# Optimization experiments

Measured on AMD Instinct MI355X. Metric: run time of the kernel, lower is better.

Reference implementation:

```python
import jax, jax.numpy as jnp
import numpy as np

N_NODES = 50000
N_EDGES = 800000
N_GRAPHS = 50
N_OBS = 4
N_FEAT = 64
N_LAYERS = 3


def setup_inputs() -> dict:
    key = jax.random.key(0)
    ks = jax.random.split(key, 12)
    x = jax.random.normal(ks[0], (N_NODES, N_OBS), dtype=jnp.float32)
    # every node appears at least once as a target (col) so degree > 0 everywhere
    row = jax.random.randint(ks[1], (N_EDGES,), 0, N_NODES, dtype=jnp.int32)
    col = jnp.concatenate([
        jnp.arange(N_NODES, dtype=jnp.int32),
        jax.random.randint(ks[2], (N_EDGES - N_NODES,), 0, N_NODES, dtype=jnp.int32),
    ])
    edge_index = jnp.stack([row, col])  # [2, E]
    batch = jnp.repeat(jnp.arange(N_GRAPHS, dtype=jnp.int32), N_NODES // N_GRAPHS)

    def w(k, shape):
        fan_in = shape[0]
        return jax.random.normal(k, shape, dtype=jnp.float32) / jnp.sqrt(jnp.float32(fan_in))

    return {
        "x": x,
        "W_init": w(ks[3], (N_OBS, N_FEAT)),
        "W_e1": w(ks[4], (N_OBS, N_FEAT - 1)),
        "W_e2": w(ks[5], (N_FEAT, N_FEAT)),
        "W_msg": w(ks[6], (N_LAYERS, 2 * N_FEAT, N_FEAT)),
        "W_upd": w(ks[7], (N_LAYERS, 2 * N_FEAT, N_FEAT)),
        "W_pool": w(ks[8], (N_FEAT, N_FEAT)),
        "W_read": w(ks[9], (2 * N_FEAT, 1)),
        "b_read": jnp.zeros((1,), dtype=jnp.float32),
        "edge_index": edge_index,
        "batch": batch,
        "batch_size": N_GRAPHS,
    }


def reference(x, W_init, W_e1, W_e2, W_msg, W_upd, W_pool, W_read, b_read,
              edge_index, batch, batch_size):
    n = x.shape[0]
    row, col = edge_index[0], edge_index[1]
    # in-degree at target nodes (PyG degree(col, N))
    deg = jax.ops.segment_sum(jnp.ones_like(col, dtype=x.dtype), col, num_segments=n)
    deg_inv = (1.0 / deg)[:, None]  # [N,1]

    # node init embedding
    cur = jax.nn.relu(x @ W_init)  # [N,F]

    # EdgeAndNodeEmbeddingLayer
    h = jax.nn.relu(x @ W_e1)  # [N,F-1]
    agg = deg_inv * jax.ops.segment_sum(h[row], col, num_segments=n)  # [N,F-1]
    y = jnp.concatenate([agg, (deg / deg.max())[:, None]], axis=1)  # [N,F]
    edge_emb = jax.nn.relu(y @ W_e2)  # [N,F]

    # UpdateNodeEmbeddingLayer x n_layers
    for i in range(W_msg.shape[0]):
        nagg = deg_inv * jax.ops.segment_sum(cur[row], col, num_segments=n)
        msg = jax.nn.relu(jnp.concatenate([nagg, edge_emb], axis=-1) @ W_msg[i])
        cur = jax.nn.relu(jnp.concatenate([cur, msg], axis=-1) @ W_upd[i])

    # ReadoutLayer (graphs are equal-sized, batch is sorted -> means[batch])
    counts = jax.ops.segment_sum(jnp.ones((n,), dtype=x.dtype), batch, num_segments=batch_size)
    means = jax.ops.segment_sum(cur, batch, num_segments=batch_size) / counts[:, None]
    global_pool = means[batch]  # [N,F]
    f_pooled = global_pool @ W_pool
    features = jax.nn.relu(jnp.concatenate([f_pooled, cur], axis=-1))  # [N,2F]
    out = features @ W_read + b_read  # [N,1]
    return out
```

## Files before the change

### kernel.cpp

```cpp
#include <hip/hip_runtime.h>
#include <hip/hip_bf16.h>

#define N_NODES 50000
#define N_EDGES 800000
#define NF      64
#define NG      50
#define NPG     (N_NODES / NG)
#define SCAN_NBLK ((N_NODES + 255) / 256)
#define MCHUNK  20
#define MROWS   (NPG / MCHUNK)
#define NTILES  (N_NODES / 16)
#define GATHER_BLKS ((NTILES + 3) / 4)
#define INIT_BLKS ((N_NODES * 32 + 255) / 256)
#define NBKT ((N_NODES + 255) / 256)
#define BKT_CAP 6144
#define P1_EPB 4096
#define P1_BLKS ((N_EDGES + P1_EPB - 1) / P1_EPB)

typedef __attribute__((ext_vector_type(8))) short bf16x8;
typedef __attribute__((ext_vector_type(4))) float f32x4;
typedef unsigned short u16;
typedef unsigned char u8;

__device__ inline unsigned pkbf(float a, float b) {
    unsigned ua = __float_as_uint(a) + 0x8000u;
    unsigned ub = __float_as_uint(b) + 0x8000u;
    return (ua >> 16) | (ub & 0xFFFF0000u);
}
__device__ inline short bf1(float a) {
    return (short)((__float_as_uint(a) + 0x8000u) >> 16);
}
__device__ inline float lo2f(unsigned u) { return __uint_as_float(u << 16); }
__device__ inline float hi2f(unsigned u) { return __uint_as_float(u & 0xFFFF0000u); }
__device__ inline void accp(float2* a, uint4 v) {
    a[0].x += lo2f(v.x); a[0].y += hi2f(v.x);
    a[1].x += lo2f(v.y); a[1].y += hi2f(v.y);
    a[2].x += lo2f(v.z); a[2].y += hi2f(v.z);
    a[3].x += lo2f(v.w); a[3].y += hi2f(v.w);
}

__global__ void k_bucket_init(const int* __restrict__ row, const int* __restrict__ col,
                              int* __restrict__ bktCnt, unsigned* __restrict__ bktData,
                              const float* __restrict__ x, const float* __restrict__ Wi,
                              const float* __restrict__ We1,
                              u16* __restrict__ cur, u16* __restrict__ h) {
    if (blockIdx.x < P1_BLKS) {
        __shared__ int lh[256], lbase[256];
        int t = threadIdx.x;
        lh[t] = 0;
        __syncthreads();
        int e0 = blockIdx.x * P1_EPB;
        int myb[16], myr[16];
        unsigned mypk[16];
#pragma unroll
        for (int i = 0; i < 16; i++) {
            int e = e0 + i * 256 + t;
            myb[i] = -1;
            if (e < N_EDGES) {
                int c = col[e];
                mypk[i] = ((unsigned)c << 16) | (unsigned)row[e];
                int b = c >> 8;
                myb[i] = b;
                myr[i] = atomicAdd(&lh[b], 1);
            }
        }
        __syncthreads();
        if (lh[t] > 0) lbase[t] = atomicAdd(&bktCnt[t], lh[t]);
        __syncthreads();
#pragma unroll
        for (int i = 0; i < 16; i++)
            if (myb[i] >= 0)
                bktData[(size_t)myb[i] * BKT_CAP + lbase[myb[i]] + myr[i]] = mypk[i];
        return;
    }
    int idx = (blockIdx.x - P1_BLKS) * 256 + threadIdx.x;
    int node = idx >> 5, q = idx & 31;
    if (node >= N_NODES) return;
    int f0 = 2 * q, f1 = 2 * q + 1;
    float4 xv = ((const float4*)x)[node];
    float c0 = xv.x * Wi[f0] + xv.y * Wi[64 + f0] + xv.z * Wi[128 + f0] + xv.w * Wi[192 + f0];
    float c1 = xv.x * Wi[f1] + xv.y * Wi[64 + f1] + xv.z * Wi[128 + f1] + xv.w * Wi[192 + f1];
    ((unsigned*)cur)[node * 32 + q] = pkbf(fmaxf(c0, 0.f), fmaxf(c1, 0.f));
    float h0 = xv.x * We1[f0] + xv.y * We1[63 + f0] + xv.z * We1[126 + f0] + xv.w * We1[189 + f0];
    h0 = fmaxf(h0, 0.f);
    float h1 = 0.f;
    if (f1 < 63) {
        h1 = xv.x * We1[f1] + xv.y * We1[63 + f1] + xv.z * We1[126 + f1] + xv.w * We1[189 + f1];
        h1 = fmaxf(h1, 0.f);
    }
    ((unsigned*)h)[node * 32 + q] = pkbf(h0, h1);
}

__global__ __launch_bounds__(256) void k_bsort(
        const unsigned* __restrict__ bktData, const int* __restrict__ bktCnt,
        int* __restrict__ deg, int* __restrict__ rowptr, u16* __restrict__ csr) {
    int b = blockIdx.x, t = threadIdx.x;
    int cnt = bktCnt[b];
    int p = (t < b) ? bktCnt[t] : 0;
    for (int off = 32; off; off >>= 1) p += __shfl_xor(p, off, 64);
    __shared__ int sr[4];
    if ((t & 63) == 0) sr[t >> 6] = p;
    __shared__ int lh[256];
    lh[t] = 0;
    __syncthreads();
    int prev = sr[0] + sr[1] + sr[2] + sr[3];
    const unsigned* bd = bktData + (size_t)b * BKT_CAP;
    for (int i = t; i < cnt; i += 256)
        atomicAdd(&lh[(bd[i] >> 16) & 255], 1);
    __syncthreads();
    int myh = lh[t];
    __shared__ int s[256];
    s[t] = myh;
    __syncthreads();
    for (int off = 1; off < 256; off <<= 1) {
        int u = (t >= off) ? s[t - off] : 0;
        __syncthreads();
        s[t] += u;
        __syncthreads();
    }
    __shared__ int lof[256];
    lof[t] = s[t] - myh;
    int node = b * 256 + t;
    if (node < N_NODES) { deg[node] = myh; rowptr[node] = prev + lof[t]; }
    if (b == 0 && t == 0) rowptr[N_NODES] = N_EDGES;
    __shared__ int cur[256];
    cur[t] = 0;
    __syncthreads();
    for (int i = t; i < cnt; i += 256) {
        unsigned pk = bd[i];
        int ln = (pk >> 16) & 255;
        int pos = atomicAdd(&cur[ln], 1);
        csr[prev + lof[ln] + pos] = (u16)(pk & 0xFFFFu);
    }
}

__global__ void k_blocksum(const int* __restrict__ deg,
                           int* __restrict__ dmax, int* __restrict__ hist) {
    __shared__ int lh[256];
    int t = threadIdx.x;
    lh[t] = 0;
    __syncthreads();
    int i = blockIdx.x * 256 + t;
    int d = (i < N_NODES) ? deg[i] : 0;
    if (i < N_NODES) atomicAdd(&lh[min(d, 255)], 1);
    int m = d;
    for (int off = 32; off; off >>= 1) m = max(m, __shfl_xor(m, off, 64));
    if ((t & 63) == 0) atomicMax(dmax, m);
    __syncthreads();
    if (lh[t]) atomicAdd(&hist[t], lh[t]);
}

__global__ __launch_bounds__(256) void k_permsort(
        const int* __restrict__ deg, const int* __restrict__ hist,
        int* __restrict__ binBump, int* __restrict__ perm) {
    int b = blockIdx.x, t = threadIdx.x;
    __shared__ int lh[256], lbase[256];
    lh[t] = 0;
    __syncthreads();
    int i = b * 256 + t;
    int v = (i < N_NODES) ? deg[i] : 0;
    int bin = min(v, 255);
    int rank = 0;
    if (i < N_NODES) rank = atomicAdd(&lh[bin], 1);
    __shared__ int s[256];
    int hv = hist[t];
    s[t] = hv;
    __syncthreads();
    for (int off = 1; off < 256; off <<= 1) {
        int u = (t >= off) ? s[t - off] : 0;
        __syncthreads();
        s[t] += u;
        __syncthreads();
    }
    int total = s[255];
    int hpref = total - s[t];
    if (lh[t] > 0) lbase[t] = hpref + atomicAdd(&binBump[t], lh[t]);
    __syncthreads();
    if (i < N_NODES) perm[lbase[bin] + rank] = i;
}

__device__ inline void gather_tile(const u16* __restrict__ src,
                                   const int* __restrict__ rowptr,
                                   const u16* __restrict__ csr,
                                   int node, int m, int q, int wv,
                                   short (*AT)[16][64]) {
    int beg = rowptr[node], end = rowptr[node + 1];
    float2 ac[8];
#pragma unroll
    for (int i = 0; i < 8; i++) ac[i] = make_float2(0.f, 0.f);
    int j = beg;
    for (; j + 5 < end; j += 6) {
        int r0 = csr[j],     r1 = csr[j + 1], r2 = csr[j + 2];
        int r3 = csr[j + 3], r4 = csr[j + 4], r5 = csr[j + 5];
        const uint4* p0 = (const uint4*)(src + (size_t)r0 * 64 + q * 16);
        const uint4* p1 = (const uint4*)(src + (size_t)r1 * 64 + q * 16);
        const uint4* p2 = (const uint4*)(src + (size_t)r2 * 64 + q * 16);
        const uint4* p3 = (const uint4*)(src + (size_t)r3 * 64 + q * 16);
        const uint4* p4 = (const uint4*)(src + (size_t)r4 * 64 + q * 16);
        const uint4* p5 = (const uint4*)(src + (size_t)r5 * 64 + q * 16);
        uint4 v00 = p0[0], v01 = p0[1];
        uint4 v10 = p1[0], v11 = p1[1];
        uint4 v20 = p2[0], v21 = p2[1];
        uint4 v30 = p3[0], v31 = p3[1];
        uint4 v40 = p4[0], v41 = p4[1];
        uint4 v50 = p5[0], v51 = p5[1];
        accp(ac, v00); accp(ac + 4, v01);
        accp(ac, v10); accp(ac + 4, v11);
        accp(ac, v20); accp(ac + 4, v21);
        accp(ac, v30); accp(ac + 4, v31);
        accp(ac, v40); accp(ac + 4, v41);
        accp(ac, v50); accp(ac + 4, v51);
    }
    for (; j + 3 < end; j += 4) {
        int r0 = csr[j], r1 = csr[j + 1], r2 = csr[j + 2], r3 = csr[j + 3];
        const uint4* p0 = (const uint4*)(src + (size_t)r0 * 64 + q * 16);
        const uint4* p1 = (const uint4*)(src + (size_t)r1 * 64 + q * 16);
        const uint4* p2 = (const uint4*)(src + (size_t)r2 * 64 + q * 16);
        const uint4* p3 = (const uint4*)(src + (size_t)r3 * 64 + q * 16);
        uint4 v00 = p0[0], v01 = p0[1];
        uint4 v10 = p1[0], v11 = p1[1];
        uint4 v20 = p2[0], v21 = p2[1];
        uint4 v30 = p3[0], v31 = p3[1];
        accp(ac, v00); accp(ac + 4, v01);
        accp(ac, v10); accp(ac + 4, v11);
        accp(ac, v20); accp(ac + 4, v21);
        accp(ac, v30); accp(ac + 4, v31);
    }
    for (; j < end; j++) {
        int r = csr[j];
        const uint4* p = (const uint4*)(src + (size_t)r * 64 + q * 16);
        uint4 v0 = p[0], v1 = p[1];
        accp(ac, v0); accp(ac + 4, v1);
    }
    float inv = 1.0f / (float)(end - beg);
    uint4 lo, hi;
    lo.x = pkbf(ac[0].x * inv, ac[0].y * inv);
    lo.y = pkbf(ac[1].x * inv, ac[1].y * inv);
    lo.z = pkbf(ac[2].x * inv, ac[2].y * inv);
    lo.w = pkbf(ac[3].x * inv, ac[3].y * inv);
    hi.x = pkbf(ac[4].x * inv, ac[4].y * inv);
    hi.y = pkbf(ac[5].x * inv, ac[5].y * inv);
    hi.z = pkbf(ac[6].x * inv, ac[6].y * inv);
    hi.w = pkbf(ac[7].x * inv, ac[7].y * inv);
    *(uint4*)&AT[wv][m][((2 * q) ^ (m & 7)) * 8]     = lo;
    *(uint4*)&AT[wv][m][((2 * q + 1) ^ (m & 7)) * 8] = hi;
}

__global__ __launch_bounds__(256) void k_edge_f(
        const u16* __restrict__ h, const int* __restrict__ rowptr,
        const u16* __restrict__ csr, const int* __restrict__ dmax,
        const float* __restrict__ We2, const int* __restrict__ perm,
        u16* __restrict__ ee) {
    __shared__ unsigned SB[2][4][64][4];
    __shared__ short AT[4][16][64];
    int t = threadIdx.x;
    for (int F = t; F < 512; F += 256) {
        int ks = F >> 8, tile = (F >> 6) & 3, ln = F & 63;
        int c = ln & 15, qq = ln >> 4;
        const float* W = We2 + (ks * 32 + qq * 8) * 64 + tile * 16 + c;
        unsigned d0 = pkbf(W[0],       W[64]);
        unsigned d1 = pkbf(W[2 * 64],  W[3 * 64]);
        unsigned d2 = pkbf(W[4 * 64],  W[5 * 64]);
        unsigned d3 = pkbf(W[6 * 64],  W[7 * 64]);
        int slot = ln ^ ((ln >> 3) & 7);
        SB[ks][tile][slot][0] = d0; SB[ks][tile][slot][1] = d1;
        SB[ks][tile][slot][2] = d2; SB[ks][tile][slot][3] = d3;
    }
    __syncthreads();
    int wv = t >> 6, lane = t & 63;
    int m = lane & 15, quad = lane >> 4;
    int slot = lane ^ ((lane >> 3) & 7);
    float idm = 1.0f / (float)dmax[0];
    for (int tb = blockIdx.x * 4 + wv; tb < NTILES; tb += gridDim.x * 4) {
        int base = tb * 16;
        int pn = perm[base + m];
        gather_tile(h, rowptr, csr, pn, m, quad, wv, AT);
        float dv = (float)(rowptr[pn + 1] - rowptr[pn]) * idm;
        int prw[4];
#pragma unroll
        for (int r = 0; r < 4; r++) prw[r] = perm[base + quad * 4 + r];
        f32x4 acc[4];
#pragma unroll
        for (int i = 0; i < 4; i++) acc[i] = (f32x4){0.f, 0.f, 0.f, 0.f};
#pragma unroll
        for (int ks = 0; ks < 2; ks++) {
            int gp = (ks * 4 + quad) ^ (m & 7);
            bf16x8 a = *(const bf16x8*)&AT[wv][m][gp * 8];
            if (ks == 1 && quad == 3) a[7] = bf1(dv);
#pragma unroll
            for (int tile = 0; tile < 4; tile++) {
                bf16x8 b = *(const bf16x8*)&SB[ks][tile][slot][0];
                acc[tile] = __builtin_amdgcn_mfma_f32_16x16x32_bf16(a, b, acc[tile], 0, 0, 0);
            }
        }
#pragma unroll
        for (int tile = 0; tile < 4; tile++)
#pragma unroll
            for (int r = 0; r < 4; r++)
                ee[(size_t)prw[r] * 64 + tile * 16 + m] =
                    (u16)bf1(fmaxf(acc[tile][r], 0.f));
    }
}

template <bool F32OUT>
__global__ __launch_bounds__(256) void k_flayer(
        const u16* __restrict__ cur, const u16* __restrict__ ee,
        const int* __restrict__ rowptr, const u16* __restrict__ csr,
        const float* __restrict__ Wm, const float* __restrict__ Wu,
        const int* __restrict__ perm, void* __restrict__ outp) {
    __shared__ unsigned SB[2][4][4][64][4];
    __shared__ short XT[4][16][64];
    int t = threadIdx.x;
    for (int F = t; F < 2048; F += 256) {
        int g = F >> 10, ks = (F >> 8) & 3, tile = (F >> 6) & 3, ln = F & 63;
        int c = ln & 15, qq = ln >> 4;
        const float* W = (g ? Wu : Wm) + (ks * 32 + qq * 8) * 64 + tile * 16 + c;
        unsigned d0 = pkbf(W[0],      W[64]);
        unsigned d1 = pkbf(W[2 * 64], W[3 * 64]);
        unsigned d2 = pkbf(W[4 * 64], W[5 * 64]);
        unsigned d3 = pkbf(W[6 * 64], W[7 * 64]);
        int slot = ln ^ ((ln >> 3) & 7);
        SB[g][ks][tile][slot][0] = d0; SB[g][ks][tile][slot][1] = d1;
        SB[g][ks][tile][slot][2] = d2; SB[g][ks][tile][slot][3] = d3;
    }
    __syncthreads();
    int wv = t >> 6, lane = t & 63;
    int m = lane & 15, quad = lane >> 4;
    int slot = lane ^ ((lane >> 3) & 7);
    for (int tb = blockIdx.x * 4 + wv; tb < NTILES; tb += gridDim.x * 4) {
        int base = tb * 16;
        int pn = perm[base + m];
        gather_tile(cur, rowptr, csr, pn, m, quad, wv, XT);
        const u16* erow = ee  + (size_t)pn * 64;
        const u16* crow = cur + (size_t)pn * 64;
        int prw[4];
#pragma unroll
        for (int r = 0; r < 4; r++) prw[r] = perm[base + quad * 4 + r];
        f32x4 acc[4];
#pragma unroll
        for (int i = 0; i < 4; i++) acc[i] = (f32x4){0.f, 0.f, 0.f, 0.f};
#pragma unroll
        for (int ks = 0; ks < 4; ks++) {
            bf16x8 a;
            if (ks < 2) {
                int gp = (ks * 4 + quad) ^ (m & 7);
                a = *(const bf16x8*)&XT[wv][m][gp * 8];
            } else {
                a = *(const bf16x8*)(erow + (ks - 2) * 32 + quad * 8);
            }
#pragma unroll
            for (int tile = 0; tile < 4; tile++) {
                bf16x8 b = *(const bf16x8*)&SB[0][ks][tile][slot][0];
                acc[tile] = __builtin_amdgcn_mfma_f32_16x16x32_bf16(a, b, acc[tile], 0, 0, 0);
            }
        }
#pragma unroll
        for (int tile = 0; tile < 4; tile++)
#pragma unroll
            for (int r = 0; r < 4; r++) {
                int node = quad * 4 + r;
                int f = tile * 16 + m;
                int sidx = (((f >> 3) ^ (node & 7)) << 3) | (f & 7);
                XT[wv][node][sidx] = bf1(fmaxf(acc[tile][r], 0.f));
            }
#pragma unroll
        for (int i = 0; i < 4; i++) acc[i] = (f32x4){0.f, 0.f, 0.f, 0.f};
#pragma unroll
        for (int ks = 0; ks < 4; ks++) {
            bf16x8 a;
            if (ks < 2) {
                a = *(const bf16x8*)(crow + ks * 32 + quad * 8);
            } else {
                int gp = ((ks - 2) * 4 + quad) ^ (m & 7);
                a = *(const bf16x8*)&XT[wv][m][gp << 3];
            }
#pragma unroll
            for (int tile = 0; tile < 4; tile++) {
                bf16x8 b = *(const bf16x8*)&SB[1][ks][tile][slot][0];
                acc[tile] = __builtin_amdgcn_mfma_f32_16x16x32_bf16(a, b, acc[tile], 0, 0, 0);
            }
        }
#pragma unroll
        for (int tile = 0; tile < 4; tile++)
#pragma unroll
            for (int r = 0; r < 4; r++) {
                float v = fmaxf(acc[tile][r], 0.f);
                size_t oi = (size_t)prw[r] * 64 + tile * 16 + m;
                if (F32OUT) ((float*)outp)[oi] = v;
                else        ((u16*)outp)[oi] = (u16)bf1(v);
            }
    }
}

__global__ __launch_bounds__(256) void k_means2(const float* __restrict__ cur,
                                                float* __restrict__ pmeans) {
    int g = blockIdx.x / MCHUNK;
    int c = blockIdx.x % MCHUNK;
    int t = threadIdx.x, f = t & 63, q = t >> 6;
    int base = g * NPG + c * MROWS;
    float acc = 0.f;
    for (int n = base + q; n < base + MROWS; n += 4) acc += cur[(size_t)n * 64 + f];
    __shared__ float red[4][64];
    red[q][f] = acc;
    __syncthreads();
    if (q == 0)
        pmeans[(size_t)(g * MCHUNK + c) * 64 + f] =
            red[0][f] + red[1][f] + red[2][f] + red[3][f];
}

__global__ __launch_bounds__(256) void k_pool2(
        const float* __restrict__ pmeans, const float* __restrict__ Wp,
        const float* __restrict__ Wr, float* __restrict__ r1) {
    __shared__ float sm[4][64];
    int wv = threadIdx.x >> 6, lane = threadIdx.x & 63;
    for (int g = wv; g < NG; g += 4) {
        float m = 0.f;
        const float* pm = pmeans + (size_t)g * MCHUNK * 64 + lane;
#pragma unroll
        for (int c = 0; c < MCHUNK; c++) m += pm[c * 64];
        sm[wv][lane] = m * (1.0f / NPG);
        float a2 = 0.f;
#pragma unroll 16
        for (int k = 0; k < 64; k++) a2 = fmaf(sm[wv][k], Wp[k * 64 + lane], a2);
        float v = fmaxf(a2, 0.f) * Wr[lane];
        for (int off = 32; off; off >>= 1) v += __shfl_xor(v, off, 64);
        if (lane == 0) r1[g] = v;
    }
}

__global__ void k_read2(const float* __restrict__ cur, const float* __restrict__ r1,
                        const int* __restrict__ batch, const float* __restrict__ Wr,
                        const float* __restrict__ br, float* __restrict__ out) {
    int idx = blockIdx.x * 256 + threadIdx.x;
    int node = idx >> 4;
    if (node >= N_NODES) return;
    int q = idx & 15;
    float4 c = *(const float4*)(cur + (size_t)node * 64 + q * 4);
    float4 w = *(const float4*)(Wr + 64 + q * 4);
    float v = fmaxf(c.x, 0.f) * w.x + fmaxf(c.y, 0.f) * w.y
            + fmaxf(c.z, 0.f) * w.z + fmaxf(c.w, 0.f) * w.w;
    v += __shfl_xor(v, 1, 64); v += __shfl_xor(v, 2, 64);
    v += __shfl_xor(v, 4, 64); v += __shfl_xor(v, 8, 64);
    if (q == 0) out[node] = v + r1[batch[node]] + br[0];
}

extern "C" void kernel_launch(void* const* d_in, const int* in_sizes, int n_in,
                              void* d_out, int out_size, void* d_ws, size_t ws_size,
                              hipStream_t stream) {
    const float* x    = (const float*)d_in[0];
    const float* Wi   = (const float*)d_in[1];
    const float* We1  = (const float*)d_in[2];
    const float* We2  = (const float*)d_in[3];
    const float* Wm   = (const float*)d_in[4];
    const float* Wu   = (const float*)d_in[5];
    const float* Wp   = (const float*)d_in[6];
    const float* Wr   = (const float*)d_in[7];
    const float* br   = (const float*)d_in[8];
    const int*   ei   = (const int*)d_in[9];
    const int*   batch= (const int*)d_in[10];
    const int* row = ei;
    const int* col = ei + N_EDGES;
    float* out = (float*)d_out;

    char* w = (char*)d_ws;
    size_t off = 0;
    auto carve = [&](size_t bytes) -> void* {
        void* p = (void*)(w + off);
        off += (bytes + 255) & ~(size_t)255;
        return p;
    };
    int*   dmax     = (int*)carve(256);
    int*   hist     = (int*)carve(256 * 4);
    int*   binBump  = (int*)carve(256 * 4);
    int*   bktCnt   = (int*)carve(256 * 4);
    size_t zero_span = off;
    unsigned* bktData = (unsigned*)carve((size_t)NBKT * BKT_CAP * 4);
    int*   deg      = (int*)carve((size_t)N_NODES * 4);
    int*   rowptr   = (int*)carve((size_t)(N_NODES + 1) * 4);
    u16*   csr      = (u16*)carve((size_t)N_EDGES * 2);
    int*   perm     = (int*)carve((size_t)N_NODES * 4);
    float* pmeans   = (float*)carve((size_t)NG * MCHUNK * 64 * 4);
    u16*   bufA     = (u16*)carve((size_t)N_NODES * 64 * 2);
    u16*   bufB     = (u16*)carve((size_t)N_NODES * 64 * 2);
    u16*   ee       = (u16*)carve((size_t)N_NODES * 64 * 2);
    float* curF     = (float*)carve((size_t)N_NODES * 64 * 4);
    float* r1       = (float*)carve((size_t)NG * 4);

    hipMemsetAsync(d_ws, 0, zero_span, stream);

    k_bucket_init<<<P1_BLKS + INIT_BLKS, 256, 0, stream>>>(row, col, bktCnt, bktData,
                                                           x, Wi, We1, bufA, bufB);
    k_bsort   <<<NBKT, 256, 0, stream>>>(bktData, bktCnt, deg, rowptr, csr);
    k_blocksum<<<SCAN_NBLK, 256, 0, stream>>>(deg, dmax, hist);
    k_permsort<<<SCAN_NBLK, 256, 0, stream>>>(deg, hist, binBump, perm);

    k_edge_f<<<GATHER_BLKS, 256, 0, stream>>>(bufB, rowptr, csr, dmax, We2, perm, ee);

    k_flayer<false><<<GATHER_BLKS, 256, 0, stream>>>(bufA, ee, rowptr, csr,
                                                     Wm, Wu, perm, bufB);
    k_flayer<false><<<GATHER_BLKS, 256, 0, stream>>>(bufB, ee, rowptr, csr,
                                                     Wm + 128 * 64, Wu + 128 * 64,
                                                     perm, bufA);
    k_flayer<true> <<<GATHER_BLKS, 256, 0, stream>>>(bufA, ee, rowptr, csr,
                                                     Wm + 2 * 128 * 64, Wu + 2 * 128 * 64,
                                                     perm, curF);

    k_means2<<<NG * MCHUNK, 256, 0, stream>>>(curF, pmeans);
    k_pool2 <<<1, 256, 0, stream>>>(pmeans, Wp, Wr, r1);
    k_read2<<<(N_NODES * 16 + 255) / 256, 256, 0, stream>>>(curF, r1, batch, Wr, br, out);
}
```

Measured before the change: 262.1 us.

## Fuse degree histogram into bucket sort and sort CSR neighbors in LDS

Folds the k_blocksum work (max degree and degree histogram) into k_bsort, removing one kernel launch and one pass over deg. The CSR scatter now goes into a shared-memory staging buffer. Each node's neighbor list is then insertion-sorted by source index and written out with coalesced stores, which should improve gather locality in the later layers. The per-thread insertion sort adds serial work that grows with degree, and the larger shared-memory footprint may reduce occupancy.

```diff
diff --git a/kernel.cpp b/kernel.cpp
--- a/kernel.cpp
+++ b/kernel.cpp
@@ -93,15 +93,16 @@
 
 __global__ __launch_bounds__(256) void k_bsort(
         const unsigned* __restrict__ bktData, const int* __restrict__ bktCnt,
-        int* __restrict__ deg, int* __restrict__ rowptr, u16* __restrict__ csr) {
+        int* __restrict__ deg, int* __restrict__ rowptr, u16* __restrict__ csr,
+        int* __restrict__ dmax, int* __restrict__ hist) {
     int b = blockIdx.x, t = threadIdx.x;
     int cnt = bktCnt[b];
     int p = (t < b) ? bktCnt[t] : 0;
     for (int off = 32; off; off >>= 1) p += __shfl_xor(p, off, 64);
     __shared__ int sr[4];
     if ((t & 63) == 0) sr[t >> 6] = p;
-    __shared__ int lh[256];
-    lh[t] = 0;
+    __shared__ int lh[256], hh[256];
+    lh[t] = 0; hh[t] = 0;
     __syncthreads();
     int prev = sr[0] + sr[1] + sr[2] + sr[3];
     const unsigned* bd = bktData + (size_t)b * BKT_CAP;
@@ -109,6 +110,11 @@
         atomicAdd(&lh[(bd[i] >> 16) & 255], 1);
     __syncthreads();
     int myh = lh[t];
+    int node = b * 256 + t;
+    int mm = myh;
+    for (int off = 32; off; off >>= 1) mm = max(mm, __shfl_xor(mm, off, 64));
+    if ((t & 63) == 0) atomicMax(dmax, mm);
+    if (node < N_NODES) atomicAdd(&hh[min(myh, 255)], 1);
     __shared__ int s[256];
     s[t] = myh;
     __syncthreads();
@@ -120,34 +126,32 @@
     }
     __shared__ int lof[256];
     lof[t] = s[t] - myh;
-    int node = b * 256 + t;
     if (node < N_NODES) { deg[node] = myh; rowptr[node] = prev + lof[t]; }
     if (b == 0 && t == 0) rowptr[N_NODES] = N_EDGES;
-    __shared__ int cur[256];
-    cur[t] = 0;
+    if (hh[t]) atomicAdd(&hist[t], hh[t]);
+    __shared__ int curs[256];
+    curs[t] = 0;
+    __shared__ u16 csr_l[BKT_CAP];
     __syncthreads();
     for (int i = t; i < cnt; i += 256) {
         unsigned pk = bd[i];
         int ln = (pk >> 16) & 255;
-        int pos = atomicAdd(&cur[ln], 1);
-        csr[prev + lof[ln] + pos] = (u16)(pk & 0xFFFFu);
-    }
-}
-
-__global__ void k_blocksum(const int* __restrict__ deg,
-                           int* __restrict__ dmax, int* __restrict__ hist) {
-    __shared__ int lh[256];
-    int t = threadIdx.x;
-    lh[t] = 0;
-    __syncthreads();
-    int i = blockIdx.x * 256 + t;
-    int d = (i < N_NODES) ? deg[i] : 0;
-    if (i < N_NODES) atomicAdd(&lh[min(d, 255)], 1);
-    int m = d;
-    for (int off = 32; off; off >>= 1) m = max(m, __shfl_xor(m, off, 64));
-    if ((t & 63) == 0) atomicMax(dmax, m);
-    __syncthreads();
-    if (lh[t]) atomicAdd(&hist[t], lh[t]);
+        int pos = atomicAdd(&curs[ln], 1);
+        csr_l[lof[ln] + pos] = (u16)(pk & 0xFFFFu);
+    }
+    __syncthreads();
+    int base = lof[t];
+    for (int i = 1; i < myh; i++) {
+        u16 key = csr_l[base + i];
+        int j = i - 1;
+        while (j >= 0 && csr_l[base + j] > key) {
+            csr_l[base + j + 1] = csr_l[base + j];
+            j--;
+        }
+        csr_l[base + j + 1] = key;
+    }
+    __syncthreads();
+    for (int i = t; i < cnt; i += 256) csr[prev + i] = csr_l[i];
 }
 
 __global__ __launch_bounds__(256) void k_permsort(
@@ -490,8 +494,8 @@
 
     k_bucket_init<<<P1_BLKS + INIT_BLKS, 256, 0, stream>>>(row, col, bktCnt, bktData,
                                                            x, Wi, We1, bufA, bufB);
-    k_bsort   <<<NBKT, 256, 0, stream>>>(bktData, bktCnt, deg, rowptr, csr);
-    k_blocksum<<<SCAN_NBLK, 256, 0, stream>>>(deg, dmax, hist);
+    k_bsort   <<<NBKT, 256, 0, stream>>>(bktData, bktCnt, deg, rowptr, csr,
+                                         dmax, hist);
     k_permsort<<<SCAN_NBLK, 256, 0, stream>>>(deg, hist, binBump, perm);
 
     k_edge_f<<<GATHER_BLKS, 256, 0, stream>>>(bufB, rowptr, csr, dmax, We2, perm, ee);
```

Measured after the change: 292.3 us. +11.5%, slower.
